# Kernel tuning notes

Hardware: AMD Instinct MI355X
Metric: run time of the kernel (lower is better)

Reference implementation:

```python
import jax, jax.numpy as jnp
import numpy as np

B, T, E, H = 32, 512, 768, 512
P_CLASSES, C_CLASSES = 5, 3


def _lstm_cell(x, h, c, Wih, Whh, bih, bhh):
    # PyTorch gate ordering: i, f, g, o
    gates = x @ Wih.T + bih + h @ Whh.T + bhh  # [B, 4H]
    i, f, g, o = jnp.split(gates, 4, axis=-1)
    c2 = jax.nn.sigmoid(f) * c + jax.nn.sigmoid(i) * jnp.tanh(g)
    h2 = jax.nn.sigmoid(o) * jnp.tanh(c2)
    return h2, c2


def _run_direction(embeds, enc_proj, Wih, Whh, bih, bhh, dec_W, dec_b, v, reverse):
    # embeds: [B,T,E], enc_proj: [B,T,H] (time-invariant encoder projection, hoisted)
    xs = jnp.swapaxes(embeds, 0, 1)  # [T,B,E]
    if reverse:
        xs = xs[::-1]
    h0 = jnp.zeros((embeds.shape[0], dec_W.shape[0]), embeds.dtype)

    def step(carry, x_t):
        h, c = carry
        dec = h @ dec_W.T + dec_b                                   # [B,H]
        scores = jnp.einsum('h,bth->bt', v, jnp.tanh(enc_proj + dec[:, None, :]))
        w = jax.nn.softmax(scores, axis=1)                          # [B,T]
        ctx = jnp.einsum('bt,bte->be', w, embeds)                   # [B,E]
        inp = jnp.concatenate([ctx, x_t], axis=1)                   # [B,2E]
        h2, c2 = _lstm_cell(inp, h, c, Wih, Whh, bih, bhh)
        return (h2, c2), h2

    _, hs = jax.lax.scan(step, (h0, h0), xs)  # hs: [T,B,H]
    if reverse:
        hs = hs[::-1]
    return jnp.swapaxes(hs, 0, 1)  # [B,T,H]


def setup_inputs() -> dict:
    key = jax.random.key(0)
    ks = jax.random.split(key, 20)
    k_lstm = 1.0 / np.sqrt(H)
    u = lambda k, shape, b: jax.random.uniform(k, shape, jnp.float32, -b, b)
    return {
        'sentence_embeds': jax.random.normal(ks[0], (B, T, E), jnp.float32),
        'Wih_f': u(ks[1], (4 * H, 2 * E), k_lstm), 'Whh_f': u(ks[2], (4 * H, H), k_lstm),
        'bih_f': u(ks[3], (4 * H,), k_lstm), 'bhh_f': u(ks[4], (4 * H,), k_lstm),
        'Wih_b': u(ks[5], (4 * H, 2 * E), k_lstm), 'Whh_b': u(ks[6], (4 * H, H), k_lstm),
        'bih_b': u(ks[7], (4 * H,), k_lstm), 'bhh_b': u(ks[8], (4 * H,), k_lstm),
        'enc_W': u(ks[9], (H, E), 1.0 / np.sqrt(E)), 'enc_b': u(ks[10], (H,), 1.0 / np.sqrt(E)),
        'dec_W': u(ks[11], (H, H), k_lstm), 'dec_b': u(ks[12], (H,), k_lstm),
        'v': jax.random.uniform(ks[13], (H,), jnp.float32, 0.0, 1.0),
        'para_W': u(ks[14], (P_CLASSES, 2 * H), 1.0 / np.sqrt(2 * H)),
        'para_b': u(ks[15], (P_CLASSES,), 1.0 / np.sqrt(2 * H)),
        'chap_W': u(ks[16], (C_CLASSES, 2 * H), 1.0 / np.sqrt(2 * H)),
        'chap_b': u(ks[17], (C_CLASSES,), 1.0 / np.sqrt(2 * H)),
    }


def reference(sentence_embeds, Wih_f, Whh_f, bih_f, bhh_f, Wih_b, Whh_b, bih_b, bhh_b,
              enc_W, enc_b, dec_W, dec_b, v, para_W, para_b, chap_W, chap_b):
    # Time-invariant encoder attention projection (original recomputes it each step; same math)
    enc_proj = sentence_embeds @ enc_W.T + enc_b  # [B,T,H]
    fwd = _run_direction(sentence_embeds, enc_proj, Wih_f, Whh_f, bih_f, bhh_f,
                         dec_W, dec_b, v, reverse=False)
    bwd = _run_direction(sentence_embeds, enc_proj, Wih_b, Whh_b, bih_b, bhh_b,
                         dec_W, dec_b, v, reverse=True)
    comb = jnp.concatenate([fwd, bwd], axis=-1)  # [B,T,2H]
    para = comb @ para_W.T + para_b              # [B,T,P]
    chap = comb @ chap_W.T + chap_b              # [B,T,C]
    return jnp.concatenate([para, chap], axis=-1)  # [B,T,P+C]
```

## Files before the change

kernel.cpp:

```cpp
#include <hip/hip_runtime.h>
#include <stdint.h>

#define Bz 32
#define Tz 512
#define Ez 768
#define Hz 512
#define G4 2048
#define AK 1536
#define NBLK 256
#define NSTEP 512

typedef __attribute__((ext_vector_type(8))) short short8;
typedef __attribute__((ext_vector_type(4))) float f32x4;

#define OFF_SUB    0u
#define OFF_GRP    1024u
#define OFF_FLAGS  2048u
#define OFF_TOP    3072u
#define OFF_AMATH  3136u
#define OFF_AMATL  199744u
#define OFF_HPH    396352u
#define OFF_HPL    527424u
#define CTRL_BYTES 658496u
#define OFF_DEC    658496u
#define OFF_PSTAT  789568u
#define OFF_BIASG  793664u
#define OFF_PCTX   810048u
#define OFF_EMB16  2382912u
#define OFF_EP32   27548736u
#define OFF_WIH    61103168u
#define OFF_WHH    73686080u
#define OFF_WENCHI OFF_AMATH
#define OFF_WENCLO OFF_PCTX
#define WS_NEEDED  77880384u

__device__ __forceinline__ float b2f(short s){
  union { unsigned int u; float f; } w;
  w.u = ((unsigned int)(unsigned short)s) << 16;
  return w.f;
}
__device__ __forceinline__ unsigned short f2b(float f){
  union { float f; unsigned int u; } w; w.f = f;
  unsigned int u = w.u;
  return (unsigned short)((u + 0x7fffu + ((u >> 16) & 1u)) >> 16);
}
__device__ __forceinline__ unsigned int pk(float x){
  const unsigned short h = f2b(x);
  const unsigned short l = f2b(x - b2f((short)h));
  return ((unsigned int)h << 16) | (unsigned int)l;
}
__device__ __forceinline__ float fast_tanh(float x){
  float e = __expf(2.f * x);
  return 1.f - 2.f / (e + 1.f);
}
__device__ __forceinline__ float sigf(float x){
  return 1.f / (1.f + __expf(-x));
}
__device__ __forceinline__ float wsum(float v){
  #pragma unroll
  for (int o = 32; o > 0; o >>= 1) v += __shfl_xor(v, o, 64);
  return v;
}
__device__ __forceinline__ float wmaxr(float v){
  #pragma unroll
  for (int o = 32; o > 0; o >>= 1) v = fmaxf(v, __shfl_xor(v, o, 64));
  return v;
}

__device__ __forceinline__ unsigned int ald32(const unsigned int* p){
  return __hip_atomic_load(p, __ATOMIC_RELAXED, __HIP_MEMORY_SCOPE_AGENT);
}
__device__ __forceinline__ float ald32f(const float* p){
  return __hip_atomic_load(p, __ATOMIC_RELAXED, __HIP_MEMORY_SCOPE_AGENT);
}
__device__ __forceinline__ unsigned long long ald64(const unsigned long long* p){
  return __hip_atomic_load(p, __ATOMIC_RELAXED, __HIP_MEMORY_SCOPE_AGENT);
}
__device__ __forceinline__ void ast32(unsigned int* p, unsigned int v){
  __hip_atomic_store(p, v, __ATOMIC_RELAXED, __HIP_MEMORY_SCOPE_AGENT);
}
__device__ __forceinline__ void ast32f(float* p, float v){
  __hip_atomic_store(p, v, __ATOMIC_RELAXED, __HIP_MEMORY_SCOPE_AGENT);
}
__device__ __forceinline__ short8 ald8s(const unsigned short* p){
  union { unsigned long long u[2]; short8 s; } w;
  const unsigned long long* q = (const unsigned long long*)p;
  w.u[0] = ald64(q);
  w.u[1] = ald64(q + 1);
  return w.s;
}

__device__ __forceinline__ void gbar_arrive(unsigned int* sub, unsigned int* top,
                                            unsigned int* flags, unsigned int bk,
                                            int blk, int tid){
  if (tid == 0){
    const unsigned int o =
        __hip_atomic_fetch_add(sub + (unsigned)(blk >> 3) * 8u, 1u,
                               __ATOMIC_RELAXED, __HIP_MEMORY_SCOPE_AGENT);
    if (o == 8u * bk - 1u){
      const unsigned int t =
          __hip_atomic_fetch_add(top, 1u, __ATOMIC_RELAXED,
                                 __HIP_MEMORY_SCOPE_AGENT);
      if (t == 32u * bk - 1u){
        #pragma unroll
        for (int i = 0; i < 32; ++i)
          __hip_atomic_store(flags + i * 8, bk, __ATOMIC_RELAXED,
                             __HIP_MEMORY_SCOPE_AGENT);
      }
    }
  }
}
__device__ __forceinline__ void gbar_wait(unsigned int* flags, unsigned int bk,
                                          int blk, int tid){
  if (tid == 0){
    while (__hip_atomic_load(flags + (unsigned)(blk >> 3) * 8u,
                             __ATOMIC_RELAXED, __HIP_MEMORY_SCOPE_AGENT) < bk)
      __builtin_amdgcn_s_sleep(2);
  }
  __syncthreads();
}

__device__ __forceinline__ void gsync(unsigned int* grp, int b,
                                      unsigned int gk, int tid){
  __syncthreads();
  if (tid == 0){
    __hip_atomic_fetch_add(grp + (unsigned)b * 8u, 1u,
                           __ATOMIC_RELAXED, __HIP_MEMORY_SCOPE_AGENT);
    while (__hip_atomic_load(grp + (unsigned)b * 8u, __ATOMIC_RELAXED,
                             __HIP_MEMORY_SCOPE_AGENT) < 8u * gk)
      __builtin_amdgcn_s_sleep(1);
  }
  __syncthreads();
}

__global__ void cvtk(const float* __restrict__ src, unsigned short* __restrict__ dst, int n){
  int i = blockIdx.x * blockDim.x + threadIdx.x;
  const int stride = gridDim.x * blockDim.x;
  for (; i < n; i += stride) dst[i] = f2b(src[i]);
}

__global__ void splitk(const float* __restrict__ src, unsigned short* __restrict__ hi,
                       unsigned short* __restrict__ lo, int n){
  int i = blockIdx.x * blockDim.x + threadIdx.x;
  const int stride = gridDim.x * blockDim.x;
  for (; i < n; i += stride){
    const float x = src[i];
    const unsigned short h = f2b(x);
    hi[i] = h;
    lo[i] = f2b(x - b2f((short)h));
  }
}

__global__ void biask(const float* bihf, const float* bhhf,
                      const float* bihb, const float* bhhb, float* bg){
  int i = blockIdx.x * blockDim.x + threadIdx.x;
  if (i < G4) bg[i] = bihf[i] + bhhf[i];
  else if (i < 2 * G4) bg[i] = bihb[i - G4] + bhhb[i - G4];
}

__global__ void outinit(float* out, const float* parab, const float* chapb){
  const int i = blockIdx.x * blockDim.x + threadIdx.x;
  if (i < Bz * Tz * 8){
    const int c = i & 7;
    out[i] = (c < 5) ? parab[c] : chapb[c - 5];
  }
}

__global__ __launch_bounds__(256, 1) void encgemm(
    const float* __restrict__ embf,
    const unsigned short* __restrict__ wenchi, const unsigned short* __restrict__ wenclo,
    const float* __restrict__ encb, float* __restrict__ ep32)
{
  const int lane = threadIdx.x & 63, wvv = threadIdx.x >> 6;
  const int mt = blockIdx.x * 4 + wvv;
  const int m0 = mt * 16;
  const int n = lane & 15, quad = lane >> 4;
  f32x4 acc[32];
  #pragma unroll
  for (int i = 0; i < 32; ++i) acc[i] = (f32x4){0.f, 0.f, 0.f, 0.f};
  const float* ar = embf + ((size_t)(m0 + n)) * Ez;
  for (int kk = 0; kk < 24; ++kk){
    const int k = kk * 32 + quad * 8;
    const f32x4 a0 = *(const f32x4*)(ar + k);
    const f32x4 a1 = *(const f32x4*)(ar + k + 4);
    short8 ah, al;
    #pragma unroll
    for (int j = 0; j < 4; ++j){
      unsigned short h0 = f2b(a0[j]);
      ah[j] = (short)h0; al[j] = (short)f2b(a0[j] - b2f((short)h0));
      unsigned short h1 = f2b(a1[j]);
      ah[4 + j] = (short)h1; al[4 + j] = (short)f2b(a1[j] - b2f((short)h1));
    }
    #pragma unroll
    for (int nt = 0; nt < 32; ++nt){
      const size_t bo = ((size_t)(nt * 16 + n)) * Ez + k;
      const short8 bh = *(const short8*)(wenchi + bo);
      const short8 bl = *(const short8*)(wenclo + bo);
      acc[nt] = __builtin_amdgcn_mfma_f32_16x16x32_bf16(ah, bh, acc[nt], 0, 0, 0);
      acc[nt] = __builtin_amdgcn_mfma_f32_16x16x32_bf16(ah, bl, acc[nt], 0, 0, 0);
      acc[nt] = __builtin_amdgcn_mfma_f32_16x16x32_bf16(al, bh, acc[nt], 0, 0, 0);
    }
  }
  #pragma unroll
  for (int nt = 0; nt < 32; ++nt){
    const int colg = nt * 16 + n;
    const float bb = encb[colg];
    #pragma unroll
    for (int r = 0; r < 4; ++r){
      const int row = m0 + quad * 4 + r;
      ep32[(size_t)row * Hz + colg] = acc[nt][r] + bb;
    }
  }
}

__global__ __launch_bounds__(1024) void scan_kernel(
    unsigned int* sub, unsigned int* top, unsigned int* flags, unsigned int* grp,
    unsigned short* amathi, unsigned short* amatlo,
    unsigned short* hph, unsigned short* hpl,
    float* decw, float* pctx, float* pstat,
    const float* __restrict__ biasg,
    const float* __restrict__ embf, const unsigned short* __restrict__ emb16,
    const float* __restrict__ ep32,
    const unsigned short* __restrict__ wih16, const unsigned short* __restrict__ whh16,
    const float* __restrict__ decWf, const float* __restrict__ decbias,
    const float* __restrict__ vvec,
    const float* __restrict__ paraW, const float* __restrict__ chapW,
    float* __restrict__ out)
{
  __shared__ unsigned short emb16s[64 * 768];
  __shared__ float hs[1024];
  __shared__ float red[2112];
  __shared__ float decs[1024];
  __shared__ float scs[2][64];
  __shared__ float pw[2][64];
  __shared__ float fac[2][8];
  __shared__ float gateval[512];

  const int blk = blockIdx.x;
  const int tid = threadIdx.x;
  const int lane = tid & 63, wv = tid >> 6;

  const int d_dir = blk >> 7, mhalf = (blk >> 6) & 1, s4d = blk & 63;
  const int b_b = blk >> 3, b_q = blk & 7;
  const int t0 = b_q * 64;

  {
    const unsigned int* src32 =
        (const unsigned int*)(emb16 + ((size_t)(b_b * Tz + t0)) * Ez);
    unsigned int* dst32 = (unsigned int*)emb16s;
    for (int i = tid; i < 24576; i += 1024) dst32[i] = src32[i];
  }
  float vr[8];
  #pragma unroll
  for (int j = 0; j < 8; ++j) vr[j] = vvec[j * 64 + lane];

  const int dn = lane & 15, dquad = lane >> 4;
  short8 Bfrag[4][2];
  #pragma unroll
  for (int kk = 0; kk < 4; ++kk){
    const int k = wv * 128 + kk * 32 + dquad * 8;
    #pragma unroll
    for (int j = 0; j < 2; ++j){
      const int coln = ((dn >> 2) * 512) + s4d * 8 + j * 4 + (dn & 3);
      Bfrag[kk][j] = (k < 1536)
        ? *(const short8*)(wih16 + ((size_t)(d_dir * G4) + coln) * 1536 + k)
        : *(const short8*)(whh16 + ((size_t)(d_dir * G4) + coln) * 512 + (k - 1536));
    }
  }
  float wreg[32];
  {
    const float* wrow = decWf + ((size_t)(b_q * 64 + (tid >> 4))) * Hz + (tid & 15);
    #pragma unroll
    for (int i = 0; i < 32; ++i) wreg[i] = wrow[i * 16];
  }
  float db_r = 0.f;
  if (tid < 128) db_r = decbias[b_q * 64 + (tid & 63)];

  float wcp[8];
  {
    const int c8 = wv >> 1, half = wv & 1;
    const float* Wrow = (c8 < 5) ? (paraW + (size_t)c8 * 1024)
                                 : (chapW + (size_t)(c8 - 5) * 1024);
    #pragma unroll
    for (int i = 0; i < 8; ++i) wcp[i] = Wrow[half * 512 + i * 64 + lane];
  }

  const int p_lb = tid >> 3, p_u = tid & 7;
  const int p_jh = s4d * 8 + p_u;
  const int p_batch = mhalf * 16 + (p_lb & 15);
  float bgi = 0.f, bgf = 0.f, bgg = 0.f, bgo = 0.f;
  float creg = 0.f;
  if (tid < 128){
    bgi = biasg[d_dir * G4 + p_jh];
    bgf = biasg[d_dir * G4 + 512 + p_jh];
    bgg = biasg[d_dir * G4 + 1024 + p_jh];
    bgo = biasg[d_dir * G4 + 1536 + p_jh];
  }

  const int abatch = mhalf * 16 + dn;

  unsigned int bk = 0, gk = 0;

  for (int s = 0; s < NSTEP; ++s){
    const int par = s & 1;
    {
      if (tid < 512){
        const int dir = tid >> 8, cw = tid & 255;
        const unsigned int wb = (((unsigned)par * 2 + dir) * Bz + b_b) * 256u + cw;
        const unsigned int hiw = ald32(((const unsigned int*)hph) + wb);
        const unsigned int low = ald32(((const unsigned int*)hpl) + wb);
        hs[dir * 512 + 2 * cw]     = b2f((short)(hiw & 0xffffu)) + b2f((short)(low & 0xffffu));
        hs[dir * 512 + 2 * cw + 1] = b2f((short)(hiw >> 16))     + b2f((short)(low >> 16));
      } else if (tid < 608){
        const int i2 = tid - 512;
        const int dir = i2 / 48, p = i2 % 48;
        const int e = b_q * 96 + 2 * p;
        const int ts = dir ? (Tz - 1 - s) : s;
        const float x0 = embf[((size_t)(b_b * Tz + ts)) * Ez + e];
        const float x1 = embf[((size_t)(b_b * Tz + ts)) * Ez + e + 1];
        const unsigned int u0 = pk(x0), u1 = pk(x1);
        const unsigned wi = (((unsigned)(dir * Bz + b_b)) * AK + 768u + (unsigned)e) >> 1;
        ast32(((unsigned int*)amathi) + wi, (u0 >> 16) | (u1 & 0xffff0000u));
        ast32(((unsigned int*)amatlo) + wi, (u0 & 0xffffu) | ((u1 & 0xffffu) << 16));
      }
      __syncthreads();
      {
        const int kc = tid & 15, j2 = tid >> 4;
        float a0 = 0.f, a1 = 0.f;
        #pragma unroll
        for (int i = 0; i < 32; ++i){
          a0 += hs[kc + i * 16] * wreg[i];
          a1 += hs[512 + kc + i * 16] * wreg[i];
        }
        red[kc * 132 + j2] = a0;
        red[kc * 132 + 66 + j2] = a1;
      }
      __syncthreads();
      if (tid < 128){
        const int dir = tid >> 6, j2 = tid & 63;
        float ssum = 0.f;
        #pragma unroll
        for (int i = 0; i < 16; ++i) ssum += red[i * 132 + dir * 66 + j2];
        ast32f(decw + ((size_t)(dir * Bz + b_b)) * Hz + b_q * 64 + j2, ssum + db_r);
      }
      __syncthreads();
      ++gk;
      if (tid == 0)
        __hip_atomic_fetch_add(grp + (unsigned)b_b * 8u, 1u,
                               __ATOMIC_RELAXED, __HIP_MEMORY_SCOPE_AGENT);
      if (s > 0 && b_q == (s & 7)){
        const int half = wv & 1, c8 = wv >> 1;
        float vv = 0.f;
        #pragma unroll
        for (int i = 0; i < 8; ++i)
          vv += hs[half * 512 + i * 64 + lane] * wcp[i];
        vv = wsum(vv);
        if (lane == 0){
          const int ts = half ? (Tz - s) : (s - 1);
          float* po = out + ((size_t)(b_b * Tz + ts)) * 8 + c8;
          ast32f(po, ald32f(po) + vv);
        }
      }
      if (tid == 0){
        while (__hip_atomic_load(grp + (unsigned)b_b * 8u, __ATOMIC_RELAXED,
                                 __HIP_MEMORY_SCOPE_AGENT) < 8u * gk)
          __builtin_amdgcn_s_sleep(1);
      }
      __syncthreads();

      decs[tid] = ald32f(decw + (((size_t)(tid >> 9)) * Bz + b_b) * Hz + (tid & 511));
      __syncthreads();
      float dff[8], dfb[8];
      #pragma unroll
      for (int j = 0; j < 8; ++j){
        dff[j] = decs[j * 64 + lane];
        dfb[j] = decs[512 + j * 64 + lane];
      }
      #pragma unroll 1
      for (int i = 0; i < 4; ++i){
        const int tl = wv * 4 + i;
        const float* er = ep32 + ((size_t)(b_b * Tz + t0 + tl)) * Hz;
        float ev[8];
        #pragma unroll
        for (int j = 0; j < 8; ++j) ev[j] = er[j * 64 + lane];
        float sf = 0.f, sb = 0.f;
        #pragma unroll
        for (int j = 0; j < 8; ++j){
          sf += vr[j] * fast_tanh(ev[j] + dff[j]);
          sb += vr[j] * fast_tanh(ev[j] + dfb[j]);
        }
        sf = wsum(sf); sb = wsum(sb);
        if (lane == 0){ scs[0][tl] = sf; scs[1][tl] = sb; }
      }
      __syncthreads();
      if (wv < 2){
        const float sv = scs[wv][lane];
        const float m = wmaxr(sv);
        const float p = __expf(sv - m);
        const float l = wsum(p);
        pw[wv][lane] = p;
        if (lane == 0){
          ast32f(pstat + (((wv * Bz) + b_b) * 8 + b_q) * 2 + 0, m);
          ast32f(pstat + (((wv * Bz) + b_b) * 8 + b_q) * 2 + 1, l);
        }
      }
      __syncthreads();
      if (lane < 24){
        const int e2 = wv * 24 + lane;
        const unsigned int* s32 = (const unsigned int*)emb16s;
        float aF0 = 0.f, aF1 = 0.f, aB0 = 0.f, aB1 = 0.f;
        #pragma unroll 8
        for (int t = 0; t < 64; ++t){
          const unsigned int u = s32[t * 384 + e2];
          const float x0 = b2f((short)(u & 0xffffu));
          const float x1 = b2f((short)(u >> 16));
          const float w0 = pw[0][t], w1 = pw[1][t];
          aF0 += w0 * x0; aF1 += w0 * x1;
          aB0 += w1 * x0; aB1 += w1 * x1;
        }
        const int e = 2 * e2;
        float* p0 = pctx + ((size_t)(0 * Bz + b_b) * 8 + b_q) * Ez + e;
        float* p1 = pctx + ((size_t)(1 * Bz + b_b) * 8 + b_q) * Ez + e;
        ast32f(p0, aF0); ast32f(p0 + 1, aF1);
        ast32f(p1, aB0); ast32f(p1 + 1, aB1);
      }
      ++gk; gsync(grp, b_b, gk, tid);

      if (tid < 16){
        const int dir = tid >> 3, qq = tid & 7;
        const float m = ald32f(pstat + (((dir * Bz) + b_b) * 8 + qq) * 2 + 0);
        const float l = ald32f(pstat + (((dir * Bz) + b_b) * 8 + qq) * 2 + 1);
        float M = m;
        #pragma unroll
        for (int o = 1; o < 8; o <<= 1) M = fmaxf(M, __shfl_xor(M, o, 8));
        const float term = l * __expf(m - M);
        float L = term;
        #pragma unroll
        for (int o = 1; o < 8; o <<= 1) L += __shfl_xor(L, o, 8);
        fac[dir][qq] = __expf(m - M) / L;
      }
      __syncthreads();
      if (tid < 96){
        const int dir = tid / 48, p = tid % 48;
        const int e = b_q * 96 + 2 * p;
        float s0 = 0.f, s1 = 0.f;
        #pragma unroll
        for (int qq = 0; qq < 8; ++qq){
          const float fq = fac[dir][qq];
          const float* pb = pctx + ((size_t)(dir * Bz + b_b) * 8 + qq) * Ez + e;
          s0 += ald32f(pb) * fq;
          s1 += ald32f(pb + 1) * fq;
        }
        const unsigned int u0 = pk(s0), u1 = pk(s1);
        const unsigned wi = (((unsigned)(dir * Bz + b_b)) * AK + (unsigned)e) >> 1;
        ast32(((unsigned int*)amathi) + wi, (u0 >> 16) | (u1 & 0xffff0000u));
        ast32(((unsigned int*)amatlo) + wi, (u0 & 0xffffu) | ((u1 & 0xffffu) << 16));
      }
    }
    ++bk;
    __syncthreads();
    gbar_arrive(sub, top, flags, bk, blk, tid);
    if (tid < 512) gateval[tid] = 0.f;
    gbar_wait(flags, bk, blk, tid);

    {
      const int dir = d_dir;
      f32x4 C0 = {0.f, 0.f, 0.f, 0.f}, C1 = {0.f, 0.f, 0.f, 0.f};
      if (wv < 12){
        const size_t arow = ((size_t)(dir * Bz) + abatch) * AK;
        #pragma unroll
        for (int kk = 0; kk < 4; ++kk){
          const int k = wv * 128 + kk * 32 + dquad * 8;
          const short8 Ah = ald8s(amathi + arow + k);
          const short8 Al = ald8s(amatlo + arow + k);
          C0 = __builtin_amdgcn_mfma_f32_16x16x32_bf16(Ah, Bfrag[kk][0], C0, 0, 0, 0);
          C0 = __builtin_amdgcn_mfma_f32_16x16x32_bf16(Al, Bfrag[kk][0], C0, 0, 0, 0);
          C1 = __builtin_amdgcn_mfma_f32_16x16x32_bf16(Ah, Bfrag[kk][1], C1, 0, 0, 0);
          C1 = __builtin_amdgcn_mfma_f32_16x16x32_bf16(Al, Bfrag[kk][1], C1, 0, 0, 0);
        }
      } else {
        const size_t hrow = (((size_t)par * 2 + dir) * Bz + abatch) * (size_t)Hz;
        #pragma unroll
        for (int kk = 0; kk < 4; ++kk){
          const int kh = (wv - 12) * 128 + kk * 32 + dquad * 8;
          const short8 Ah = ald8s(hph + hrow + kh);
          const short8 Al = ald8s(hpl + hrow + kh);
          C0 = __builtin_amdgcn_mfma_f32_16x16x32_bf16(Ah, Bfrag[kk][0], C0, 0, 0, 0);
          C0 = __builtin_amdgcn_mfma_f32_16x16x32_bf16(Al, Bfrag[kk][0], C0, 0, 0, 0);
          C1 = __builtin_amdgcn_mfma_f32_16x16x32_bf16(Ah, Bfrag[kk][1], C1, 0, 0, 0);
          C1 = __builtin_amdgcn_mfma_f32_16x16x32_bf16(Al, Bfrag[kk][1], C1, 0, 0, 0);
        }
      }
      #pragma unroll
      for (int r = 0; r < 4; ++r){
        const int rowb = (dquad * 4 + r) * 32 + (dn >> 2) * 8 + (dn & 3);
        unsafeAtomicAdd(&gateval[rowb],     C0[r]);
        unsafeAtomicAdd(&gateval[rowb + 4], C1[r]);
      }
      __syncthreads();
      if (tid < 128){
        const float gi = gateval[p_lb * 32 + p_u]       + bgi;
        const float gf = gateval[p_lb * 32 + 8 + p_u]   + bgf;
        const float gg = gateval[p_lb * 32 + 16 + p_u]  + bgg;
        const float go = gateval[p_lb * 32 + 24 + p_u]  + bgo;
        const float cnew = sigf(gf) * creg + sigf(gi) * fast_tanh(gg);
        const float hval = sigf(go) * fast_tanh(cnew);
        creg = cnew;
        const unsigned int u = pk(hval);
        const unsigned int up = __shfl_xor((int)u, 1, 64);
        if ((p_u & 1) == 0){
          const unsigned int hiw = (u >> 16) | (up & 0xffff0000u);
          const unsigned int low = (u & 0xffffu) | ((up & 0xffffu) << 16);
          const unsigned wi = ((((unsigned)(par ^ 1) * 2 + d_dir) * Bz + p_batch) * 256u)
                              + ((unsigned)p_jh >> 1);
          ast32(((unsigned int*)hph) + wi, hiw);
          ast32(((unsigned int*)hpl) + wi, low);
        }
      }
    }
    ++bk;
    __syncthreads();
    gbar_arrive(sub, top, flags, bk, blk, tid);
    gbar_wait(flags, bk, blk, tid);
  }

  if (b_q == 0){
    if (tid < 512){
      const int dir = tid >> 8, cw = tid & 255;
      const unsigned int wb = ((unsigned)dir * Bz + b_b) * 256u + cw;
      const unsigned int hiw = ald32(((const unsigned int*)hph) + wb);
      const unsigned int low = ald32(((const unsigned int*)hpl) + wb);
      hs[dir * 512 + 2 * cw]     = b2f((short)(hiw & 0xffffu)) + b2f((short)(low & 0xffffu));
      hs[dir * 512 + 2 * cw + 1] = b2f((short)(hiw >> 16))     + b2f((short)(low >> 16));
    }
    __syncthreads();
    const int half = wv & 1, c8 = wv >> 1;
    float vv = 0.f;
    #pragma unroll
    for (int i = 0; i < 8; ++i)
      vv += hs[half * 512 + i * 64 + lane] * wcp[i];
    vv = wsum(vv);
    if (lane == 0){
      const int ts = half ? 0 : (Tz - 1);
      float* po = out + ((size_t)(b_b * Tz + ts)) * 8 + c8;
      ast32f(po, ald32f(po) + vv);
    }
  }
}

extern "C" void kernel_launch(void* const* d_in, const int* in_sizes, int n_in,
                              void* d_out, int out_size, void* d_ws, size_t ws_size,
                              hipStream_t stream) {
  (void)in_sizes; (void)n_in; (void)out_size; (void)ws_size;
  const float* emb    = (const float*)d_in[0];
  const float* Wih_f  = (const float*)d_in[1];
  const float* Whh_f  = (const float*)d_in[2];
  const float* bih_f  = (const float*)d_in[3];
  const float* bhh_f  = (const float*)d_in[4];
  const float* Wih_b  = (const float*)d_in[5];
  const float* Whh_b  = (const float*)d_in[6];
  const float* bih_b  = (const float*)d_in[7];
  const float* bhh_b  = (const float*)d_in[8];
  const float* enc_W  = (const float*)d_in[9];
  const float* enc_b  = (const float*)d_in[10];
  const float* dec_W  = (const float*)d_in[11];
  const float* dec_b  = (const float*)d_in[12];
  const float* vvec   = (const float*)d_in[13];
  const float* paraW  = (const float*)d_in[14];
  const float* parab  = (const float*)d_in[15];
  const float* chapW  = (const float*)d_in[16];
  const float* chapb  = (const float*)d_in[17];
  float* out = (float*)d_out;

  uint8_t* w = (uint8_t*)d_ws;
  unsigned int* sub   = (unsigned int*)(w + OFF_SUB);
  unsigned int* grp   = (unsigned int*)(w + OFF_GRP);
  unsigned int* flags = (unsigned int*)(w + OFF_FLAGS);
  unsigned int* top   = (unsigned int*)(w + OFF_TOP);
  unsigned short* amathi = (unsigned short*)(w + OFF_AMATH);
  unsigned short* amatlo = (unsigned short*)(w + OFF_AMATL);
  unsigned short* hph    = (unsigned short*)(w + OFF_HPH);
  unsigned short* hpl    = (unsigned short*)(w + OFF_HPL);
  float* decw   = (float*)(w + OFF_DEC);
  float* pstat  = (float*)(w + OFF_PSTAT);
  float* biasg  = (float*)(w + OFF_BIASG);
  float* pctx   = (float*)(w + OFF_PCTX);
  unsigned short* emb16  = (unsigned short*)(w + OFF_EMB16);
  float* ep32   = (float*)(w + OFF_EP32);
  unsigned short* wih16 = (unsigned short*)(w + OFF_WIH);
  unsigned short* whh16 = (unsigned short*)(w + OFF_WHH);
  unsigned short* wenchi = (unsigned short*)(w + OFF_WENCHI);
  unsigned short* wenclo = (unsigned short*)(w + OFF_WENCLO);

  cvtk<<<512, 256, 0, stream>>>(Wih_f, wih16,               G4 * 2 * Ez);
  cvtk<<<512, 256, 0, stream>>>(Wih_b, wih16 + G4 * 2 * Ez, G4 * 2 * Ez);
  cvtk<<<256, 256, 0, stream>>>(Whh_f, whh16,               G4 * Hz);
  cvtk<<<256, 256, 0, stream>>>(Whh_b, whh16 + G4 * Hz,     G4 * Hz);
  splitk<<<256, 256, 0, stream>>>(enc_W, wenchi, wenclo, Hz * Ez);
  cvtk<<<1024, 256, 0, stream>>>(emb, emb16, Bz * Tz * Ez);
  biask<<<16, 256, 0, stream>>>(bih_f, bhh_f, bih_b, bhh_b, biasg);

  encgemm<<<256, 256, 0, stream>>>(emb, wenchi, wenclo, enc_b, ep32);

  hipMemsetAsync(d_ws, 0, CTRL_BYTES, stream);

  outinit<<<512, 256, 0, stream>>>(out, parab, chapb);

  scan_kernel<<<NBLK, 1024, 0, stream>>>(
      sub, top, flags, grp, amathi, amatlo, hph, hpl, decw, pctx, pstat, biasg,
      emb, emb16, ep32, wih16, whh16,
      dec_W, dec_b, vvec, paraW, chapW, out);
}
```

Baseline: 24.84 ms.

## Split grid barrier into two independent batch-half barriers and remap blocks

```diff
diff --git a/kernel.cpp b/kernel.cpp
--- a/kernel.cpp
+++ b/kernel.cpp
@@ -17,22 +17,22 @@
 #define OFF_GRP    1024u
 #define OFF_FLAGS  2048u
 #define OFF_TOP    3072u
-#define OFF_AMATH  3136u
-#define OFF_AMATL  199744u
-#define OFF_HPH    396352u
-#define OFF_HPL    527424u
-#define CTRL_BYTES 658496u
-#define OFF_DEC    658496u
-#define OFF_PSTAT  789568u
-#define OFF_BIASG  793664u
-#define OFF_PCTX   810048u
-#define OFF_EMB16  2382912u
-#define OFF_EP32   27548736u
-#define OFF_WIH    61103168u
-#define OFF_WHH    73686080u
+#define OFF_AMATH  3200u
+#define OFF_AMATL  199808u
+#define OFF_HPH    396416u
+#define OFF_HPL    527488u
+#define CTRL_BYTES 658560u
+#define OFF_DEC    658560u
+#define OFF_PSTAT  789632u
+#define OFF_BIASG  793728u
+#define OFF_PCTX   810112u
+#define OFF_EMB16  2382976u
+#define OFF_EP32   27548800u
+#define OFF_WIH    61103232u
+#define OFF_WHH    73686144u
 #define OFF_WENCHI OFF_AMATH
 #define OFF_WENCLO OFF_PCTX
-#define WS_NEEDED  77880384u
+#define WS_NEEDED  77880448u
 
 __device__ __forceinline__ float b2f(short s){
   union { unsigned int u; float f; } w;
@@ -92,28 +92,28 @@
 
 __device__ __forceinline__ void gbar_arrive(unsigned int* sub, unsigned int* top,
                                             unsigned int* flags, unsigned int bk,
-                                            int blk, int tid){
+                                            int half, int local, int tid){
   if (tid == 0){
     const unsigned int o =
-        __hip_atomic_fetch_add(sub + (unsigned)(blk >> 3) * 8u, 1u,
+        __hip_atomic_fetch_add(sub + (unsigned)(half * 16 + (local >> 3)) * 8u, 1u,
                                __ATOMIC_RELAXED, __HIP_MEMORY_SCOPE_AGENT);
     if (o == 8u * bk - 1u){
       const unsigned int t =
-          __hip_atomic_fetch_add(top, 1u, __ATOMIC_RELAXED,
+          __hip_atomic_fetch_add(top + half * 16, 1u, __ATOMIC_RELAXED,
                                  __HIP_MEMORY_SCOPE_AGENT);
-      if (t == 32u * bk - 1u){
-        #pragma unroll
-        for (int i = 0; i < 32; ++i)
-          __hip_atomic_store(flags + i * 8, bk, __ATOMIC_RELAXED,
+      if (t == 16u * bk - 1u){
+        #pragma unroll
+        for (int i = 0; i < 16; ++i)
+          __hip_atomic_store(flags + (half * 16 + i) * 8, bk, __ATOMIC_RELAXED,
                              __HIP_MEMORY_SCOPE_AGENT);
       }
     }
   }
 }
 __device__ __forceinline__ void gbar_wait(unsigned int* flags, unsigned int bk,
-                                          int blk, int tid){
+                                          int half, int local, int tid){
   if (tid == 0){
-    while (__hip_atomic_load(flags + (unsigned)(blk >> 3) * 8u,
+    while (__hip_atomic_load(flags + (unsigned)(half * 16 + (local >> 3)) * 8u,
                              __ATOMIC_RELAXED, __HIP_MEMORY_SCOPE_AGENT) < bk)
       __builtin_amdgcn_s_sleep(2);
   }
@@ -240,8 +240,9 @@
   const int tid = threadIdx.x;
   const int lane = tid & 63, wv = tid >> 6;
 
-  const int d_dir = blk >> 7, mhalf = (blk >> 6) & 1, s4d = blk & 63;
-  const int b_b = blk >> 3, b_q = blk & 7;
+  const int half = blk >> 7, local = blk & 127;
+  const int b_b = half * 16 + (local & 15), b_q = local >> 4;
+  const int d_dir = local >> 6, s4d = local & 63, mhalf = half;
   const int t0 = b_q * 64;
 
   {
@@ -278,11 +279,11 @@
 
   float wcp[8];
   {
-    const int c8 = wv >> 1, half = wv & 1;
+    const int c8 = wv >> 1, whalf = wv & 1;
     const float* Wrow = (c8 < 5) ? (paraW + (size_t)c8 * 1024)
                                  : (chapW + (size_t)(c8 - 5) * 1024);
     #pragma unroll
-    for (int i = 0; i < 8; ++i) wcp[i] = Wrow[half * 512 + i * 64 + lane];
+    for (int i = 0; i < 8; ++i) wcp[i] = Wrow[whalf * 512 + i * 64 + lane];
   }
 
   const int p_lb = tid >> 3, p_u = tid & 7;
@@ -349,14 +350,14 @@
         __hip_atomic_fetch_add(grp + (unsigned)b_b * 8u, 1u,
                                __ATOMIC_RELAXED, __HIP_MEMORY_SCOPE_AGENT);
       if (s > 0 && b_q == (s & 7)){
-        const int half = wv & 1, c8 = wv >> 1;
+        const int ohalf = wv & 1, c8 = wv >> 1;
         float vv = 0.f;
         #pragma unroll
         for (int i = 0; i < 8; ++i)
-          vv += hs[half * 512 + i * 64 + lane] * wcp[i];
+          vv += hs[ohalf * 512 + i * 64 + lane] * wcp[i];
         vv = wsum(vv);
         if (lane == 0){
-          const int ts = half ? (Tz - s) : (s - 1);
+          const int ts = ohalf ? (Tz - s) : (s - 1);
           float* po = out + ((size_t)(b_b * Tz + ts)) * 8 + c8;
           ast32f(po, ald32f(po) + vv);
         }
@@ -405,24 +406,20 @@
         }
       }
       __syncthreads();
-      if (lane < 24){
-        const int e2 = wv * 24 + lane;
+      if (lane < 48){
+        const int cdir = wv & 1, cg = wv >> 1;
+        const int e2 = cg * 48 + lane;
         const unsigned int* s32 = (const unsigned int*)emb16s;
-        float aF0 = 0.f, aF1 = 0.f, aB0 = 0.f, aB1 = 0.f;
+        float a0 = 0.f, a1 = 0.f;
         #pragma unroll 8
         for (int t = 0; t < 64; ++t){
           const unsigned int u = s32[t * 384 + e2];
-          const float x0 = b2f((short)(u & 0xffffu));
-          const float x1 = b2f((short)(u >> 16));
-          const float w0 = pw[0][t], w1 = pw[1][t];
-          aF0 += w0 * x0; aF1 += w0 * x1;
-          aB0 += w1 * x0; aB1 += w1 * x1;
-        }
-        const int e = 2 * e2;
-        float* p0 = pctx + ((size_t)(0 * Bz + b_b) * 8 + b_q) * Ez + e;
-        float* p1 = pctx + ((size_t)(1 * Bz + b_b) * 8 + b_q) * Ez + e;
-        ast32f(p0, aF0); ast32f(p0 + 1, aF1);
-        ast32f(p1, aB0); ast32f(p1 + 1, aB1);
+          const float w = pw[cdir][t];
+          a0 += w * b2f((short)(u & 0xffffu));
+          a1 += w * b2f((short)(u >> 16));
+        }
+        float* p0 = pctx + ((size_t)(cdir * Bz + b_b) * 8 + b_q) * Ez + 2 * e2;
+        ast32f(p0, a0); ast32f(p0 + 1, a1);
       }
       ++gk; gsync(grp, b_b, gk, tid);
 
@@ -459,9 +456,9 @@
     }
     ++bk;
     __syncthreads();
-    gbar_arrive(sub, top, flags, bk, blk, tid);
+    gbar_arrive(sub, top, flags, bk, half, local, tid);
     if (tid < 512) gateval[tid] = 0.f;
-    gbar_wait(flags, bk, blk, tid);
+    gbar_wait(flags, bk, half, local, tid);
 
     {
       const int dir = d_dir;
@@ -520,8 +517,8 @@
     }
     ++bk;
     __syncthreads();
-    gbar_arrive(sub, top, flags, bk, blk, tid);
-    gbar_wait(flags, bk, blk, tid);
+    gbar_arrive(sub, top, flags, bk, half, local, tid);
+    gbar_wait(flags, bk, half, local, tid);
   }
 
   if (b_q == 0){
@@ -534,14 +531,14 @@
       hs[dir * 512 + 2 * cw + 1] = b2f((short)(hiw >> 16))     + b2f((short)(low >> 16));
     }
     __syncthreads();
-    const int half = wv & 1, c8 = wv >> 1;
+    const int ohalf = wv & 1, c8 = wv >> 1;
     float vv = 0.f;
     #pragma unroll
     for (int i = 0; i < 8; ++i)
-      vv += hs[half * 512 + i * 64 + lane] * wcp[i];
+      vv += hs[ohalf * 512 + i * 64 + lane] * wcp[i];
     vv = wsum(vv);
     if (lane == 0){
-      const int ts = half ? 0 : (Tz - 1);
+      const int ts = ohalf ? 0 : (Tz - 1);
       float* po = out + ((size_t)(b_b * Tz + ts)) * 8 + c8;
       ast32f(po, ald32f(po) + vv);
     }
```

Result: faster. 23.92 ms (-3.7%).
